# Kernel optimization log

Hardware: AMD Instinct MI355X
Metric: run time of the kernel (lower is better)

Reference implementation:

```python
import jax, jax.numpy as jnp
import numpy as np

B, CH, XL, YL = 512, 1, 64, 64
H = 64                       # num_heads
D = CH * XL * YL             # 4096
F = D // H                   # feature_dim = 64 (== H, required by the mask multiply)


def setup_inputs() -> dict:
    key = jax.random.key(0)
    k1, k2, k3, k4, k5 = jax.random.split(key, 5)
    scale = 1.0 / np.sqrt(D)  # roughly kaiming-ish init for square linears
    return {
        "x": jax.random.normal(k1, (B, CH, XL, YL), dtype=jnp.float32),
        "interface_map": jax.random.uniform(k2, (B, CH, XL, YL), dtype=jnp.float32),
        "Wq": jax.random.normal(k3, (D, D), dtype=jnp.float32) * scale,
        "Wk": jax.random.normal(k4, (D, D), dtype=jnp.float32) * scale,
        "Wv": jax.random.normal(k5, (D, D), dtype=jnp.float32) * scale,
    }


def reference(x, interface_map, Wq, Wk, Wv):
    b = x.shape[0]
    xf = x.reshape(b, D)
    # nn.Linear(bias=False): y = x @ W.T
    q = (xf @ Wq.T).reshape(b, H, F)
    k = (xf @ Wk.T).reshape(b, H, F)
    v = (xf @ Wv.T).reshape(b, H, F)
    inv_sqrt_f = jnp.float32(1.0 / np.sqrt(F))
    qk_t = jnp.einsum("bhf,bgf->bhg", q, k) * inv_sqrt_f           # (B, H, H)
    qk_t = qk_t * interface_map.reshape(b, H, F)                   # multiplicative mask (F == H)
    attention_weights = jax.nn.softmax(qk_t, axis=-1)
    weighted_values = jnp.einsum("bhg,bgf->bhf", attention_weights, v)  # (B, H, F)
    combined = jnp.swapaxes(weighted_values, 1, 2).reshape(b, CH, XL, YL)
    output = x * combined
    return output, attention_weights
```

## Files before the change

kernel.cpp:

```cpp
#include <hip/hip_runtime.h>
#include <cstdint>
#include <cstddef>

typedef __attribute__((ext_vector_type(8))) short short8;
typedef __attribute__((ext_vector_type(4))) float f32x4;
typedef __attribute__((ext_vector_type(2))) unsigned int u32x2;

#define NB 512
#define DD 4096
#define NP 12288

__device__ __forceinline__ unsigned pk2(float a, float b) {
    unsigned r;
    asm("v_cvt_pk_bf16_f32 %0, %1, %2" : "=v"(r) : "v"(a), "v"(b));
    return r;
}
__device__ __forceinline__ unsigned short f2b(float a) {
    return (unsigned short)pk2(a, a);
}
__device__ __forceinline__ float2 ub2(unsigned u) {
    float2 r;
    r.x = __uint_as_float(u << 16);
    r.y = __uint_as_float(u & 0xffff0000u);
    return r;
}

__device__ __forceinline__ void gload_lds16(const void* g, void* l) {
    __builtin_amdgcn_global_load_lds((const __attribute__((address_space(1))) void*)g,
                                     (__attribute__((address_space(3))) void*)l, 16, 0, 0);
}

__global__ __launch_bounds__(256) void cvt_bf16_kernel(const float* __restrict__ src,
                                                       unsigned short* __restrict__ dst,
                                                       int n8) {
    int i = blockIdx.x * 256 + threadIdx.x;
    if (i >= n8) return;
    const float4* s = (const float4*)src + (size_t)i * 2;
    float4 a = s[0], b = s[1];
    uint4 r;
    r.x = pk2(a.x, a.y);
    r.y = pk2(a.z, a.w);
    r.z = pk2(b.x, b.y);
    r.w = pk2(b.z, b.w);
    ((uint4*)dst)[i] = r;
}

template<int KS>
__global__ __launch_bounds__(256, 3) void gemm_qkv_kernel(
    const unsigned short* __restrict__ xb,
    const float* __restrict__ w0, const float* __restrict__ w1, const float* __restrict__ w2,
    unsigned short* __restrict__ part)
{
    constexpr int KLEN = DD / KS;
    constexpr int NIT = KLEN / 32;
    constexpr int NWG = 96 * 4 * KS;
    constexpr int CPX = NWG / 8;

    const int bid = blockIdx.x;
    const int orig = (bid & 7) * CPX + (bid >> 3);
    const int nt = orig / (4 * KS);
    const int rest = orig - nt * (4 * KS);
    const int mt = rest / KS;
    const int kz = rest - mt * KS;

    const float* W = (nt < 32) ? w0 : ((nt < 64) ? w1 : w2);
    const int ntl = nt & 31;
    const unsigned short* Abase = xb + (size_t)(mt * 128) * DD + kz * KLEN;
    unsigned short* C = part + (size_t)kz * NB * NP;

    __shared__ unsigned short As[4][128 * 32];

    const int t = threadIdx.x;
    const int l = t & 63;
    const int wv = t >> 6;

    f32x4 acc[8][2];
    #pragma unroll
    for (int i = 0; i < 8; ++i)
        #pragma unroll
        for (int j = 0; j < 2; ++j)
            acc[i][j] = (f32x4){0.f, 0.f, 0.f, 0.f};

    const int arow0 = (t >> 2);
    const int acol  = (((t & 3) ^ ((t >> 3) & 3)) * 8);
    const int cx = ((l >> 4) ^ ((l >> 1) & 3));

    const float* wsrc = W + (size_t)(ntl * 128 + wv * 32 + (l & 15)) * DD + kz * KLEN + (l >> 4) * 8;

    float4 bank0[2][2], bank1[2][2];

    #define LOADB(bk, kt) { _Pragma("unroll") for (int fj = 0; fj < 2; ++fj) \
                              _Pragma("unroll") for (int h = 0; h < 2; ++h) \
                                bk[fj][h] = *(const float4*)(wsrc + (size_t)(fj * 16) * DD + (kt) * 32 + h * 4); }
    #define STAGEA(kt, buf) { _Pragma("unroll") for (int i = 0; i < 2; ++i) \
                               gload_lds16(Abase + (size_t)(i * 64 + arow0) * DD + (kt) * 32 + acol, \
                                           (char*)(&As[buf][0]) + i * 4096 + wv * 1024); }

    #define BODY(kt, BK, PF_OK, VMC) { \
        short8 bfr[2]; \
        _Pragma("unroll") for (int fj = 0; fj < 2; ++fj) { \
            union { uint4 u; short8 s; } cv; \
            cv.u.x = pk2(BK[fj][0].x, BK[fj][0].y); \
            cv.u.y = pk2(BK[fj][0].z, BK[fj][0].w); \
            cv.u.z = pk2(BK[fj][1].x, BK[fj][1].y); \
            cv.u.w = pk2(BK[fj][1].z, BK[fj][1].w); \
            bfr[fj] = cv.s; \
        } \
        if (PF_OK) { STAGEA((kt) + 2, ((kt) + 2) & 3); LOADB(BK, (kt) + 2); } \
        __builtin_amdgcn_s_setprio(1); \
        _Pragma("unroll") for (int fi = 0; fi < 8; ++fi) { \
            int row = fi * 16 + (l & 15); \
            short8 af = *(const short8*)((const char*)(&As[(kt) & 3][0]) + row * 64 + cx * 16); \
            acc[fi][0] = __builtin_amdgcn_mfma_f32_16x16x32_bf16(af, bfr[0], acc[fi][0], 0, 0, 0); \
            acc[fi][1] = __builtin_amdgcn_mfma_f32_16x16x32_bf16(af, bfr[1], acc[fi][1], 0, 0, 0); \
        } \
        __builtin_amdgcn_s_setprio(0); \
        asm volatile("s_waitcnt vmcnt(" #VMC ") lgkmcnt(0)" ::: "memory"); \
        __builtin_amdgcn_sched_barrier(0); \
        __builtin_amdgcn_s_barrier(); \
        __builtin_amdgcn_sched_barrier(0); \
    }

    STAGEA(0, 0);
    STAGEA(1, 1);
    LOADB(bank0, 0);
    LOADB(bank1, 1);
    asm volatile("s_waitcnt vmcnt(0) lgkmcnt(0)" ::: "memory");
    __builtin_amdgcn_s_barrier();
    __builtin_amdgcn_sched_barrier(0);

    for (int kt = 0; kt + 2 < NIT; kt += 2) {
        BODY(kt,     bank0, true, 6);
        BODY(kt + 1, bank1, true, 6);
    }
    BODY(NIT - 2, bank0, false, 0);
    BODY(NIT - 1, bank1, false, 0);

    #undef BODY
    #undef LOADB
    #undef STAGEA

    #pragma unroll
    for (int fi = 0; fi < 8; ++fi) {
        int rbase = mt * 128 + fi * 16 + (l >> 4) * 4;
        #pragma unroll
        for (int fj = 0; fj < 2; ++fj) {
            int col = nt * 128 + wv * 32 + fj * 16 + (l & 15);
            #pragma unroll
            for (int r = 0; r < 4; ++r) {
                unsigned short h = f2b(acc[fi][fj][r]);
                __builtin_nontemporal_store(h, &C[(size_t)(rbase + r) * NP + col]);
            }
        }
    }
}

template<int KS>
__global__ __launch_bounds__(256) void attn_kernel(
    const unsigned short* __restrict__ part,
    const float* __restrict__ x,
    const float* __restrict__ imap,
    float* __restrict__ dout)
{
    const int b = blockIdx.x;
    const int t = threadIdx.x;
    const int l = t & 63;
    const int wv = t >> 6;

    __shared__ float sq[64 * 68];
    __shared__ float sk[64 * 68];
    __shared__ float sv[64 * 68];

    const unsigned short* base0 = part + (size_t)b * NP;
    const unsigned short* base1 = part + (size_t)NB * NP + (size_t)b * NP;

    #pragma unroll
    for (int i = 0; i < 4; ++i) {
        int f4 = i * 256 + t;
        int r = f4 >> 4, c = (f4 & 15) * 4;
        u32x2 qa = __builtin_nontemporal_load((const u32x2*)(base0 + (size_t)f4 * 4));
        u32x2 ka = __builtin_nontemporal_load((const u32x2*)(base0 + DD + (size_t)f4 * 4));
        u32x2 va = __builtin_nontemporal_load((const u32x2*)(base0 + 2 * DD + (size_t)f4 * 4));
        float2 q0 = ub2(qa.x), q1 = ub2(qa.y);
        float2 k0 = ub2(ka.x), k1 = ub2(ka.y);
        float2 v0 = ub2(va.x), v1 = ub2(va.y);
        float4 q4 = {q0.x, q0.y, q1.x, q1.y};
        float4 k4 = {k0.x, k0.y, k1.x, k1.y};
        float4 v4 = {v0.x, v0.y, v1.x, v1.y};
        if (KS == 2) {
            u32x2 qb = __builtin_nontemporal_load((const u32x2*)(base1 + (size_t)f4 * 4));
            u32x2 kb = __builtin_nontemporal_load((const u32x2*)(base1 + DD + (size_t)f4 * 4));
            u32x2 vb = __builtin_nontemporal_load((const u32x2*)(base1 + 2 * DD + (size_t)f4 * 4));
            float2 a0 = ub2(qb.x), a1 = ub2(qb.y);
            float2 b0 = ub2(kb.x), b1 = ub2(kb.y);
            float2 c0 = ub2(vb.x), c1 = ub2(vb.y);
            q4.x += a0.x; q4.y += a0.y; q4.z += a1.x; q4.w += a1.y;
            k4.x += b0.x; k4.y += b0.y; k4.z += b1.x; k4.w += b1.y;
            v4.x += c0.x; v4.y += c0.y; v4.z += c1.x; v4.w += c1.y;
        }
        *(float4*)(&sq[r * 68 + c]) = q4;
        *(float4*)(&sk[r * 68 + c]) = k4;
        *(float4*)(&sv[r * 68 + c]) = v4;
    }
    __syncthreads();

    float accs[16];
    #pragma unroll
    for (int i = 0; i < 16; ++i) accs[i] = 0.f;
    #pragma unroll 4
    for (int f4 = 0; f4 < 16; ++f4) {
        float4 kvv = *(const float4*)(&sk[l * 68 + f4 * 4]);
        #pragma unroll
        for (int i = 0; i < 16; ++i) {
            int h = i * 4 + wv;
            float4 qv = *(const float4*)(&sq[h * 68 + f4 * 4]);
            accs[i] = fmaf(qv.x, kvv.x, fmaf(qv.y, kvv.y, fmaf(qv.z, kvv.z, fmaf(qv.w, kvv.w, accs[i]))));
        }
    }
    __syncthreads();
    #pragma unroll
    for (int i = 0; i < 16; ++i) {
        int h = i * 4 + wv;
        float m = imap[(size_t)b * DD + h * 64 + l];
        sk[h * 65 + l] = accs[i] * 0.125f * m;
    }
    __syncthreads();

    {
        int h = t >> 2, j = t & 3;
        float e[16];
        float mx = -3.0e38f;
        #pragma unroll
        for (int q2 = 0; q2 < 16; ++q2) {
            e[q2] = sk[h * 65 + j * 16 + q2];
            mx = fmaxf(mx, e[q2]);
        }
        mx = fmaxf(mx, __shfl_xor(mx, 1));
        mx = fmaxf(mx, __shfl_xor(mx, 2));
        float s = 0.f;
        #pragma unroll
        for (int q2 = 0; q2 < 16; ++q2) { e[q2] = __expf(e[q2] - mx); s += e[q2]; }
        s += __shfl_xor(s, 1);
        s += __shfl_xor(s, 2);
        float invs = 1.0f / s;
        float* aw = dout + (size_t)NB * DD + (size_t)b * DD + h * 64 + j * 16;
        #pragma unroll
        for (int q2 = 0; q2 < 16; q2 += 4) {
            f32x4 w4 = {e[q2] * invs, e[q2 + 1] * invs, e[q2 + 2] * invs, e[q2 + 3] * invs};
            __builtin_nontemporal_store(w4, (f32x4*)(aw + q2));
            sk[h * 65 + j * 16 + q2 + 0] = w4.x;
            sk[h * 65 + j * 16 + q2 + 1] = w4.y;
            sk[h * 65 + j * 16 + q2 + 2] = w4.z;
            sk[h * 65 + j * 16 + q2 + 3] = w4.w;
        }
    }
    __syncthreads();

    float pacc[16];
    #pragma unroll
    for (int i = 0; i < 16; ++i) pacc[i] = 0.f;
    #pragma unroll 4
    for (int g = 0; g < 64; ++g) {
        float p = sk[l * 65 + g];
        const float4* vr = (const float4*)(&sv[g * 68 + wv * 16]);
        float4 v0 = vr[0], v1 = vr[1], v2 = vr[2], v3 = vr[3];
        pacc[0]  = fmaf(p, v0.x, pacc[0]);
        pacc[1]  = fmaf(p, v0.y, pacc[1]);
        pacc[2]  = fmaf(p, v0.z, pacc[2]);
        pacc[3]  = fmaf(p, v0.w, pacc[3]);
        pacc[4]  = fmaf(p, v1.x, pacc[4]);
        pacc[5]  = fmaf(p, v1.y, pacc[5]);
        pacc[6]  = fmaf(p, v1.z, pacc[6]);
        pacc[7]  = fmaf(p, v1.w, pacc[7]);
        pacc[8]  = fmaf(p, v2.x, pacc[8]);
        pacc[9]  = fmaf(p, v2.y, pacc[9]);
        pacc[10] = fmaf(p, v2.z, pacc[10]);
        pacc[11] = fmaf(p, v2.w, pacc[11]);
        pacc[12] = fmaf(p, v3.x, pacc[12]);
        pacc[13] = fmaf(p, v3.y, pacc[13]);
        pacc[14] = fmaf(p, v3.z, pacc[14]);
        pacc[15] = fmaf(p, v3.w, pacc[15]);
    }
    const size_t ob = (size_t)b * DD + (size_t)(wv * 16) * 64 + l;
    #pragma unroll
    for (int ii = 0; ii < 16; ++ii) {
        size_t o = ob + (size_t)ii * 64;
        float r = x[o] * pacc[ii];
        __builtin_nontemporal_store(r, &dout[o]);
    }
}

extern "C" void kernel_launch(void* const* d_in, const int* in_sizes, int n_in,
                              void* d_out, int out_size, void* d_ws, size_t ws_size,
                              hipStream_t stream) {
    const float* x  = (const float*)d_in[0];
    const float* im = (const float*)d_in[1];
    const float* Wq = (const float*)d_in[2];
    const float* Wk = (const float*)d_in[3];
    const float* Wv = (const float*)d_in[4];
    float* out = (float*)d_out;

    unsigned short* xb = (unsigned short*)d_ws;
    unsigned short* part = (unsigned short*)((char*)d_ws + (size_t)NB * DD * 2);

    const size_t need2 = (size_t)NB * DD * 2 + 2ull * NB * NP * 2;
    const int KS = (ws_size >= need2) ? 2 : 1;

    cvt_bf16_kernel<<<dim3((NB * DD / 8 + 255) / 256), dim3(256), 0, stream>>>(x, xb, NB * DD / 8);

    if (KS == 2) {
        gemm_qkv_kernel<2><<<dim3(96 * 4 * 2), dim3(256), 0, stream>>>(xb, Wq, Wk, Wv, part);
        attn_kernel<2><<<dim3(NB), dim3(256), 0, stream>>>(part, x, im, out);
    } else {
        gemm_qkv_kernel<1><<<dim3(96 * 4 * 1), dim3(256), 0, stream>>>(xb, Wq, Wk, Wv, part);
        attn_kernel<1><<<dim3(NB), dim3(256), 0, stream>>>(part, x, im, out);
    }
}
```

Before: 142.7 us.

## Deepen QKV GEMM prefetch pipeline to three stages with five LDS buffers

Changes the QKV projection GEMM main loop from a two-deep to a three-deep software pipeline. A tiles now rotate through five LDS buffers and B fp32 weights through three register banks, unrolled by 15 with a compile-time tail. The aim is to hide more global-load latency on the weight stream and the activation tiles. In exchange it uses more LDS and registers, which may reduce occupancy below the launch-bounds target.

```diff
diff --git a/kernel.cpp b/kernel.cpp
--- a/kernel.cpp
+++ b/kernel.cpp
@@ -9,6 +9,8 @@
 #define NB 512
 #define DD 4096
 #define NP 12288
+
+#define SWAIT(vm) __builtin_amdgcn_s_waitcnt(((vm) & 15) | (7 << 4) | ((((vm) >> 4) & 3) << 14))
 
 __device__ __forceinline__ unsigned pk2(float a, float b) {
     unsigned r;
@@ -53,6 +55,7 @@
 {
     constexpr int KLEN = DD / KS;
     constexpr int NIT = KLEN / 32;
+    constexpr int KMAIN = ((NIT - 3) / 15) * 15;
     constexpr int NWG = 96 * 4 * KS;
     constexpr int CPX = NWG / 8;
 
@@ -68,7 +71,7 @@
     const unsigned short* Abase = xb + (size_t)(mt * 128) * DD + kz * KLEN;
     unsigned short* C = part + (size_t)kz * NB * NP;
 
-    __shared__ unsigned short As[4][128 * 32];
+    __shared__ unsigned short As[5][128 * 32];
 
     const int t = threadIdx.x;
     const int l = t & 63;
@@ -87,7 +90,7 @@
 
     const float* wsrc = W + (size_t)(ntl * 128 + wv * 32 + (l & 15)) * DD + kz * KLEN + (l >> 4) * 8;
 
-    float4 bank0[2][2], bank1[2][2];
+    float4 b0[2][2], b1[2][2], b2[2][2];
 
     #define LOADB(bk, kt) { _Pragma("unroll") for (int fj = 0; fj < 2; ++fj) \
                               _Pragma("unroll") for (int h = 0; h < 2; ++h) \
@@ -96,7 +99,7 @@
                                gload_lds16(Abase + (size_t)(i * 64 + arow0) * DD + (kt) * 32 + acol, \
                                            (char*)(&As[buf][0]) + i * 4096 + wv * 1024); }
 
-    #define BODY(kt, BK, PF_OK, VMC) { \
+    #define CORE(BUF, BK) { \
         short8 bfr[2]; \
         _Pragma("unroll") for (int fj = 0; fj < 2; ++fj) { \
             union { uint4 u; short8 s; } cv; \
@@ -106,37 +109,111 @@
             cv.u.w = pk2(BK[fj][1].z, BK[fj][1].w); \
             bfr[fj] = cv.s; \
         } \
-        if (PF_OK) { STAGEA((kt) + 2, ((kt) + 2) & 3); LOADB(BK, (kt) + 2); } \
         __builtin_amdgcn_s_setprio(1); \
         _Pragma("unroll") for (int fi = 0; fi < 8; ++fi) { \
             int row = fi * 16 + (l & 15); \
-            short8 af = *(const short8*)((const char*)(&As[(kt) & 3][0]) + row * 64 + cx * 16); \
+            short8 af = *(const short8*)((const char*)(&As[BUF][0]) + row * 64 + cx * 16); \
             acc[fi][0] = __builtin_amdgcn_mfma_f32_16x16x32_bf16(af, bfr[0], acc[fi][0], 0, 0, 0); \
             acc[fi][1] = __builtin_amdgcn_mfma_f32_16x16x32_bf16(af, bfr[1], acc[fi][1], 0, 0, 0); \
         } \
         __builtin_amdgcn_s_setprio(0); \
-        asm volatile("s_waitcnt vmcnt(" #VMC ") lgkmcnt(0)" ::: "memory"); \
+    }
+
+    #define ENDBAR(VMC) { \
+        SWAIT(VMC); \
         __builtin_amdgcn_sched_barrier(0); \
         __builtin_amdgcn_s_barrier(); \
-        __builtin_amdgcn_sched_barrier(0); \
-    }
+        __builtin_amdgcn_sched_barrier(0); }
+
+    #define ITER_M(kt, I, BK) { \
+        short8 bfr[2]; \
+        _Pragma("unroll") for (int fj = 0; fj < 2; ++fj) { \
+            union { uint4 u; short8 s; } cv; \
+            cv.u.x = pk2(BK[fj][0].x, BK[fj][0].y); \
+            cv.u.y = pk2(BK[fj][0].z, BK[fj][0].w); \
+            cv.u.z = pk2(BK[fj][1].x, BK[fj][1].y); \
+            cv.u.w = pk2(BK[fj][1].z, BK[fj][1].w); \
+            bfr[fj] = cv.s; \
+        } \
+        STAGEA((kt) + 3, ((I) + 3) % 5); \
+        LOADB(BK, (kt) + 3); \
+        __builtin_amdgcn_s_setprio(1); \
+        _Pragma("unroll") for (int fi = 0; fi < 8; ++fi) { \
+            int row = fi * 16 + (l & 15); \
+            short8 af = *(const short8*)((const char*)(&As[(I) % 5][0]) + row * 64 + cx * 16); \
+            acc[fi][0] = __builtin_amdgcn_mfma_f32_16x16x32_bf16(af, bfr[0], acc[fi][0], 0, 0, 0); \
+            acc[fi][1] = __builtin_amdgcn_mfma_f32_16x16x32_bf16(af, bfr[1], acc[fi][1], 0, 0, 0); \
+        } \
+        __builtin_amdgcn_s_setprio(0); \
+        ENDBAR(12); \
+    }
+
+    #define ITER_T(J, BK) { \
+        constexpr int kt_ = KMAIN + (J); \
+        if (kt_ < NIT) { \
+            constexpr bool PF_ = (kt_ + 3 < NIT); \
+            constexpr int VMC_ = 6 * ((kt_ + 2 < NIT) ? 1 : 0) + 6 * ((kt_ + 3 < NIT) ? 1 : 0); \
+            short8 bfr[2]; \
+            _Pragma("unroll") for (int fj = 0; fj < 2; ++fj) { \
+                union { uint4 u; short8 s; } cv; \
+                cv.u.x = pk2(BK[fj][0].x, BK[fj][0].y); \
+                cv.u.y = pk2(BK[fj][0].z, BK[fj][0].w); \
+                cv.u.z = pk2(BK[fj][1].x, BK[fj][1].y); \
+                cv.u.w = pk2(BK[fj][1].z, BK[fj][1].w); \
+                bfr[fj] = cv.s; \
+            } \
+            if (PF_) { STAGEA(kt_ + 3, ((J) + 3) % 5); LOADB(BK, kt_ + 3); } \
+            __builtin_amdgcn_s_setprio(1); \
+            _Pragma("unroll") for (int fi = 0; fi < 8; ++fi) { \
+                int row = fi * 16 + (l & 15); \
+                short8 af = *(const short8*)((const char*)(&As[(J) % 5][0]) + row * 64 + cx * 16); \
+                acc[fi][0] = __builtin_amdgcn_mfma_f32_16x16x32_bf16(af, bfr[0], acc[fi][0], 0, 0, 0); \
+                acc[fi][1] = __builtin_amdgcn_mfma_f32_16x16x32_bf16(af, bfr[1], acc[fi][1], 0, 0, 0); \
+            } \
+            __builtin_amdgcn_s_setprio(0); \
+            ENDBAR(VMC_); \
+        } }
 
     STAGEA(0, 0);
     STAGEA(1, 1);
-    LOADB(bank0, 0);
-    LOADB(bank1, 1);
-    asm volatile("s_waitcnt vmcnt(0) lgkmcnt(0)" ::: "memory");
+    STAGEA(2, 2);
+    LOADB(b0, 0);
+    LOADB(b1, 1);
+    LOADB(b2, 2);
+    SWAIT(0);
     __builtin_amdgcn_s_barrier();
     __builtin_amdgcn_sched_barrier(0);
 
-    for (int kt = 0; kt + 2 < NIT; kt += 2) {
-        BODY(kt,     bank0, true, 6);
-        BODY(kt + 1, bank1, true, 6);
-    }
-    BODY(NIT - 2, bank0, false, 0);
-    BODY(NIT - 1, bank1, false, 0);
-
-    #undef BODY
+    for (int kt0 = 0; kt0 < KMAIN; kt0 += 15) {
+        ITER_M(kt0 + 0,  0,  b0);
+        ITER_M(kt0 + 1,  1,  b1);
+        ITER_M(kt0 + 2,  2,  b2);
+        ITER_M(kt0 + 3,  3,  b0);
+        ITER_M(kt0 + 4,  4,  b1);
+        ITER_M(kt0 + 5,  5,  b2);
+        ITER_M(kt0 + 6,  6,  b0);
+        ITER_M(kt0 + 7,  7,  b1);
+        ITER_M(kt0 + 8,  8,  b2);
+        ITER_M(kt0 + 9,  9,  b0);
+        ITER_M(kt0 + 10, 10, b1);
+        ITER_M(kt0 + 11, 11, b2);
+        ITER_M(kt0 + 12, 12, b0);
+        ITER_M(kt0 + 13, 13, b1);
+        ITER_M(kt0 + 14, 14, b2);
+    }
+    ITER_T(0, b0);
+    ITER_T(1, b1);
+    ITER_T(2, b2);
+    ITER_T(3, b0);
+    ITER_T(4, b1);
+    ITER_T(5, b2);
+    ITER_T(6, b0);
+    ITER_T(7, b1);
+
+    #undef ITER_M
+    #undef ITER_T
+    #undef CORE
+    #undef ENDBAR
     #undef LOADB
     #undef STAGEA
 
```

New measurement: 141.6 us. No clear change (-0.8%).
